# Kernel tuning notes

Measured on AMD Instinct MI355X. Metric: run time of the kernel, lower is better.

Reference implementation:

```python
import jax, jax.numpy as jnp
import numpy as np

B, S, E, H = 2, 2048, 1024, 16
D = E // H  # head_dim
SCALE = 1.0 / np.sqrt(D)


def rope_tables(seq_len, dim, dtype=jnp.float32):
    # matches RotaryEmbedding: inv_freq over even indices, emb = cat([freqs, freqs])
    inv_freq = 1.0 / (10000.0 ** (jnp.arange(0, dim, 2, dtype=dtype) / dim))
    t = jnp.arange(seq_len, dtype=dtype)
    freqs = t[:, None] * inv_freq[None, :]          # [S, D/2]
    emb = jnp.concatenate([freqs, freqs], axis=-1)  # [S, D]
    return jnp.cos(emb)[None, None], jnp.sin(emb)[None, None]  # [1,1,S,D]


def apply_rope(x, cos, sin):
    # x: [B,H,S,D]; interleaved rotate exactly as the torch code:
    # x2 = stack([-x[...,1::2], x[...,0::2]], -1).reshape_as(x)
    x2 = jnp.stack([-x[..., 1::2], x[..., 0::2]], axis=-1).reshape(x.shape)
    return x * cos + x2 * sin


def setup_inputs() -> dict:
    key = jax.random.key(0)
    ks = jax.random.split(key, 12)
    std = 1.0 / np.sqrt(E)
    inp = {
        "query": jax.random.normal(ks[0], (B, S, E), jnp.float32),
        "key": jax.random.normal(ks[1], (B, S, E), jnp.float32),
        "value": jax.random.normal(ks[2], (B, S, E), jnp.float32),
        "mask": jnp.ones((B, S), jnp.int32),
        "Wq": jax.random.normal(ks[3], (E, E), jnp.float32) * std,
        "bq": jax.random.normal(ks[4], (E,), jnp.float32) * std,
        "Wk": jax.random.normal(ks[5], (E, E), jnp.float32) * std,
        "bk": jax.random.normal(ks[6], (E,), jnp.float32) * std,
        "Wv": jax.random.normal(ks[7], (E, E), jnp.float32) * std,
        "bv": jax.random.normal(ks[8], (E,), jnp.float32) * std,
        "Wo": jax.random.normal(ks[9], (E, E), jnp.float32) * std,
        "bo": jax.random.normal(ks[10], (E,), jnp.float32) * std,
    }
    return inp


def reference(query, key, value, mask, Wq, bq, Wk, bk, Wv, bv, Wo, bo):
    b, sq, _ = query.shape
    sk = key.shape[1]
    # linear projections (torch Linear: x @ W.T + b), split into heads [B,H,S,D]
    Q = (query @ Wq.T + bq).reshape(b, sq, H, D).transpose(0, 2, 1, 3)
    K = (key @ Wk.T + bk).reshape(b, sk, H, D).transpose(0, 2, 1, 3)
    V = (value @ Wv.T + bv).reshape(b, sk, H, D).transpose(0, 2, 1, 3)
    cos_q, sin_q = rope_tables(sq, D)
    cos_k, sin_k = rope_tables(sk, D)
    Q = apply_rope(Q, cos_q, sin_q)
    K = apply_rope(K, cos_k, sin_k)
    scores = jnp.einsum("bhqd,bhkd->bhqk", Q, K) * SCALE
    neg_inf = jnp.finfo(scores.dtype).min
    scores = jnp.where(mask[:, None, None, :] == 0, neg_inf, scores)
    attn = jax.nn.softmax(scores, axis=-1)
    # dropout omitted (deterministic reference / eval mode)
    out = jnp.einsum("bhqk,bhkd->bhqd", attn, V)
    out = out.transpose(0, 2, 1, 3).reshape(b, sq, E)
    return out @ Wo.T + bo
```

## Files before the change

kernel.cpp:

```cpp
#include <hip/hip_runtime.h>
#include <stdint.h>

typedef unsigned short u16;
typedef __bf16 bf16x8 __attribute__((ext_vector_type(8)));
typedef float f32x4 __attribute__((ext_vector_type(4)));
typedef float f32x2 __attribute__((ext_vector_type(2)));
typedef u16 u16x4v __attribute__((ext_vector_type(4)));

#define DI __device__ __forceinline__

constexpr int BB = 2, SS = 2048, EE = 1024, HH = 16, DD = 64;
constexpr int MROWS = BB * SS;
constexpr int KDIM = 1024, NDIM = 1024;

constexpr float FM = 12.0f;
constexpr float MNEG = -30000.f;

DI u16 f2bf(float f) {
  uint32_t u = __float_as_uint(f);
  return (u16)((u + 0x7FFFu + ((u >> 16) & 1u)) >> 16);
}
DI float bf2f(u16 h) { return __uint_as_float(((uint32_t)h) << 16); }

DI uint32_t cvtpk_bf16(float a, float b) {
  uint32_t r;
  asm("v_cvt_pk_bf16_f32 %0, %1, %2" : "=v"(r) : "v"(a), "v"(b));
  return r;
}

DI void cp16(const void* g, void* lds) {
  __builtin_amdgcn_global_load_lds((const __attribute__((address_space(1))) void*)g,
                                   (__attribute__((address_space(3))) void*)lds, 16, 0, 0);
}

DI f32x4 mfma16(bf16x8 a, bf16x8 b, f32x4 c) {
  return __builtin_amdgcn_mfma_f32_16x16x32_bf16(a, b, c, 0, 0, 0);
}

__global__ __launch_bounds__(256) void prep_cast(
    const float* __restrict__ q, const float* __restrict__ k, const float* __restrict__ v,
    const float* __restrict__ wq, const float* __restrict__ wk, const float* __restrict__ wv,
    const float* __restrict__ wo,
    u16* __restrict__ qb, u16* __restrict__ kb, u16* __restrict__ vb,
    u16* __restrict__ wqb, u16* __restrict__ wkb, u16* __restrict__ wvb,
    u16* __restrict__ wob) {
  constexpr size_t SZI = (size_t)MROWS * EE;
  constexpr size_t SZW = (size_t)EE * EE;
  const size_t g = ((size_t)blockIdx.x * 256 + threadIdx.x) * 4;
  const float* src; u16* dst; size_t o;
  if (g < SZI)          { src = q; dst = qb; o = g; }
  else if (g < 2 * SZI) { src = k; dst = kb; o = g - SZI; }
  else if (g < 3 * SZI) { src = v; dst = vb; o = g - 2 * SZI; }
  else {
    size_t t2 = g - 3 * SZI;
    int wi = (int)(t2 / SZW);
    o = t2 - (size_t)(wi < 4 ? wi : 3) * SZW;
    src = wi == 0 ? wq : wi == 1 ? wk : wi == 2 ? wv : wo;
    dst = wi == 0 ? wqb : wi == 1 ? wkb : wi == 2 ? wvb : wob;
  }
  const float4 f = *(const float4*)(src + o);
  u16x4v hv;
  hv[0] = f2bf(f.x); hv[1] = f2bf(f.y); hv[2] = f2bf(f.z); hv[3] = f2bf(f.w);
  *(u16x4v*)(dst + o) = hv;
}

__global__ __launch_bounds__(256) void rope_tables_k(float* __restrict__ csT,
                                                     const int* __restrict__ mask,
                                                     float* __restrict__ mfl) {
  const int t = blockIdx.x * 256 + threadIdx.x;
  const int s = t >> 6, d = t & 63, j = d & 31;
  const float ang = (float)s * exp2f(-(float)j * 0.4152410118f);
  float2 cs; cs.x = cosf(ang); cs.y = sinf(ang);
  ((float2*)csT)[t] = cs;
  if (t < BB * SS) mfl[t] = mask[t] ? -FM : MNEG;
}

__global__ __launch_bounds__(256) void gemm_qkv(
    const u16* __restrict__ qb, const u16* __restrict__ kb, const u16* __restrict__ vb,
    const u16* __restrict__ wqb, const u16* __restrict__ wkb, const u16* __restrict__ wvb,
    const float* __restrict__ bq, const float* __restrict__ bk, const float* __restrict__ bv,
    u16* __restrict__ Qp, u16* __restrict__ Kp, u16* __restrict__ Vtg,
    const float* __restrict__ csT) {
  __shared__ alignas(16) u16 sA[128 * 64];
  __shared__ alignas(16) u16 sB[128 * 64];
  const int tsel = blockIdx.y >> 5;
  const bool vtr = (tsel == 2);
  const u16* A    = tsel == 0 ? wqb : tsel == 1 ? wkb : vb;
  const u16* Bm   = tsel == 0 ? qb  : tsel == 1 ? kb  : wvb;
  const float* bias = tsel == 0 ? bq : tsel == 1 ? bk : bv;

  const int fBase = blockIdx.x * 128;
  const int tBase = (blockIdx.y & 31) * 128;
  const int aBase = vtr ? tBase : fBase;
  const int bBase = vtr ? fBase : tBase;
  const int tid = threadIdx.x;
  const int lane = tid & 63, w = tid >> 6;
  const int quad = lane >> 4, l16 = lane & 15;
  const int wr = w >> 1, wc = w & 1;

  size_t aSrc[4], bSrc[4];
  u16 *aDst[4], *bDst[4];
#pragma unroll
  for (int j = 0; j < 4; ++j) {
    const int c = tid + j * 256;
    const int row = c >> 3, sl = c & 7;
    const size_t off = (size_t)row * KDIM + ((sl ^ (row & 7)) * 8);
    aSrc[j] = (size_t)aBase * KDIM + off; aDst[j] = &sA[c * 8];
    bSrc[j] = (size_t)bBase * KDIM + off; bDst[j] = &sB[c * 8];
  }

  f32x4 acc[4][4];
#pragma unroll
  for (int mi = 0; mi < 4; ++mi)
#pragma unroll
    for (int ni = 0; ni < 4; ++ni)
#pragma unroll
      for (int e = 0; e < 4; ++e) acc[mi][ni][e] = 0.f;

  const int arow = wr * 64 + l16, brow = wc * 64 + l16;

  for (int k0 = 0; k0 < KDIM; k0 += 64) {
    __syncthreads();
#pragma unroll
    for (int j = 0; j < 4; ++j) {
      cp16(A + aSrc[j] + k0, aDst[j]);
      cp16(Bm + bSrc[j] + k0, bDst[j]);
    }
    __syncthreads();
#pragma unroll
    for (int h = 0; h < 2; ++h) {
      bf16x8 af[4], bf[4];
#pragma unroll
      for (int i = 0; i < 4; ++i) {
        const int ar = arow + i * 16, br = brow + i * 16;
        af[i] = *(const bf16x8*)&sA[ar * 64 + (((h * 4 + quad) ^ (ar & 7)) << 3)];
        bf[i] = *(const bf16x8*)&sB[br * 64 + (((h * 4 + quad) ^ (br & 7)) << 3)];
      }
#pragma unroll
      for (int mi = 0; mi < 4; ++mi)
#pragma unroll
        for (int ni = 0; ni < 4; ++ni)
          acc[mi][ni] = mfma16(af[mi], bf[ni], acc[mi][ni]);
    }
  }

  if (!vtr) {
    u16* C = tsel == 0 ? Qp : Kp;
#pragma unroll
    for (int mi = 0; mi < 4; ++mi) {
      const int fm = fBase + wr * 64 + mi * 16 + quad * 4;
      const float4 b4 = *(const float4*)&bias[fm];
      const int d0 = fm & 63;
#pragma unroll
      for (int ni = 0; ni < 4; ++ni) {
        const int t = tBase + wc * 64 + ni * 16 + l16;
        const int srow = t & (SS - 1);
        const float* cs = &csT[(size_t)((srow << 6) + d0) * 2];
        const float4 cs01 = *(const float4*)cs;
        const float4 cs23 = *(const float4*)(cs + 4);
        const float v0 = acc[mi][ni][0] + b4.x;
        const float v1 = acc[mi][ni][1] + b4.y;
        const float v2 = acc[mi][ni][2] + b4.z;
        const float v3 = acc[mi][ni][3] + b4.w;
        const float o0 = v0 * cs01.x - v1 * cs01.y;
        const float o1 = v1 * cs01.z + v0 * cs01.w;
        const float o2 = v2 * cs23.x - v3 * cs23.y;
        const float o3 = v3 * cs23.z + v2 * cs23.w;
        uint2 pk;
        pk.x = cvtpk_bf16(o0, o1);
        pk.y = cvtpk_bf16(o2, o3);
        *(uint2*)&C[(size_t)t * NDIM + fm] = pk;
      }
    }
  } else {
#pragma unroll
    for (int ni = 0; ni < 4; ++ni) {
      const int f = fBase + wc * 64 + ni * 16 + l16;
      const int h = f >> 6, d = f & 63;
      const float bb = bias[f];
#pragma unroll
      for (int mi = 0; mi < 4; ++mi) {
        const int t0 = tBase + wr * 64 + mi * 16 + quad * 4;
        const int b = t0 >> 11, s0 = t0 & (SS - 1);
        const int sp0 = (s0 & ~31) | (((s0 >> 2) & 3) << 3) | (((s0 >> 4) & 1) << 2);
        uint2 pk;
        pk.x = cvtpk_bf16(acc[mi][ni][0] + bb, acc[mi][ni][1] + bb);
        pk.y = cvtpk_bf16(acc[mi][ni][2] + bb, acc[mi][ni][3] + bb);
        *(uint2*)&Vtg[((size_t)((b * 16 + h) * 64 + d)) * SS + sp0] = pk;
      }
    }
  }
}

__global__ __launch_bounds__(512, 4) void attn_kernel(
    const u16* __restrict__ Qp, const u16* __restrict__ Kp, const u16* __restrict__ Vtg,
    const float* __restrict__ mfl, u16* __restrict__ Oh) {
  __shared__ alignas(16) u16 sK[2][128 * 64];
  __shared__ alignas(16) u16 sVt[2][64 * 128];
  __shared__ alignas(16) float sMaskAll[SS];
  const int tid = threadIdx.x, lane = tid & 63, w = tid >> 6;
  const int quad = lane >> 4, l16 = lane & 15;
  const int bh = blockIdx.y, b = bh >> 4, h = bh & 15;
  const int q0 = blockIdx.x * 128 + w * 16;
  const u16* Qb = Qp + (size_t)b * SS * EE + h * DD;
  const u16* Kb = Kp + (size_t)b * SS * EE + h * DD;
  const u16* Vb = Vtg + (size_t)bh * DD * SS;
  constexpr float C1 = 0.18033688011112042f;

  bf16x8 qf[2];
#pragma unroll
  for (int ks = 0; ks < 2; ++ks)
    qf[ks] = *(const bf16x8*)(Qb + (size_t)(q0 + l16) * EE + ks * 32 + quad * 8);

  f32x4 oacc[4];
#pragma unroll
  for (int nd = 0; nd < 4; ++nd)
#pragma unroll
    for (int e = 0; e < 4; ++e) oacc[nd][e] = 0.f;
  f32x2 sum2 = {0.f, 0.f};

  auto stage = [&](int kt, int bi) {
    const int key0 = kt * 128;
#pragma unroll
    for (int i = 0; i < 2; ++i) {
      const int c = i * 512 + tid;
      const int key = c >> 3;
      const int g8 = ((c & 7) ^ (key & 7)) * 8;
      cp16(Kb + (size_t)(key0 + key) * EE + g8, &sK[bi][c * 8]);
    }
#pragma unroll
    for (int i = 0; i < 2; ++i) {
      const int L = i * 512 + tid;
      const int d = L >> 4;
      const int g8 = ((L & 15) ^ (d & 15)) * 8;
      cp16(Vb + (size_t)d * SS + key0 + g8, &sVt[bi][L * 8]);
    }
  };

  auto compute = [&](int kt, int bi) {
    const int key0 = kt * 128;
    f32x4 sacc[8];
#pragma unroll
    for (int ni = 0; ni < 8; ++ni)
#pragma unroll
      for (int e = 0; e < 4; ++e) sacc[ni][e] = 0.f;
    __builtin_amdgcn_s_setprio(1);
#pragma unroll
    for (int ks = 0; ks < 2; ++ks)
#pragma unroll
      for (int ni = 0; ni < 8; ++ni) {
        const int row = ni * 16 + l16;
        const bf16x8 kf = *(const bf16x8*)&sK[bi][row * 64 + (((ks * 4 + quad) ^ (l16 & 7)) << 3)];
        sacc[ni] = mfma16(kf, qf[ks], sacc[ni]);
      }
    __builtin_amdgcn_s_setprio(0);

    uint32_t pw32[4][4];
#pragma unroll
    for (int ni = 0; ni < 8; ++ni) {
      const int kb4 = key0 + ni * 16 + quad * 4;
      const f32x2 m01 = *(const f32x2*)&sMaskAll[kb4];
      const f32x2 m23 = *(const f32x2*)&sMaskAll[kb4 + 2];
      f32x2 t01, t23;
      t01.x = sacc[ni][0]; t01.y = sacc[ni][1];
      t23.x = sacc[ni][2]; t23.y = sacc[ni][3];
      t01 = t01 * C1 + m01;
      t23 = t23 * C1 + m23;
      f32x2 p01, p23;
      p01.x = exp2f(t01.x); p01.y = exp2f(t01.y);
      p23.x = exp2f(t23.x); p23.y = exp2f(t23.y);
      sum2 += p01;
      sum2 += p23;
      const int k2 = ni >> 1, j2 = (ni & 1) * 2;
      pw32[k2][j2]     = cvtpk_bf16(p01.x, p01.y);
      pw32[k2][j2 + 1] = cvtpk_bf16(p23.x, p23.y);
    }

    __builtin_amdgcn_s_setprio(1);
#pragma unroll
    for (int k2 = 0; k2 < 4; ++k2) {
      union { uint32_t u[4]; bf16x8 v; } pf;
#pragma unroll
      for (int j = 0; j < 4; ++j) pf.u[j] = pw32[k2][j];
#pragma unroll
      for (int nd = 0; nd < 4; ++nd) {
        const int row = nd * 16 + l16;
        const bf16x8 vf = *(const bf16x8*)&sVt[bi][row * 128 + (((k2 * 4 + quad) ^ l16) << 3)];
        oacc[nd] = mfma16(pf.v, vf, oacc[nd]);
      }
    }
    __builtin_amdgcn_s_setprio(0);
  };

  stage(0, 0);
  cp16(mfl + (size_t)b * SS + tid * 4, &sMaskAll[tid * 4]);
  __syncthreads();

  for (int kt = 0; kt < SS / 128; kt += 2) {
    if (kt + 1 < SS / 128) stage(kt + 1, 1);
    compute(kt, 0);
    __syncthreads();
    if (kt + 2 < SS / 128) stage(kt + 2, 0);
    compute(kt + 1, 1);
    __syncthreads();
  }

  float lrow = sum2.x + sum2.y;
  lrow += __shfl_xor(lrow, 16, 64);
  lrow += __shfl_xor(lrow, 32, 64);
  const float linv = lrow > 0.f ? 1.0f / lrow : 0.f;

#pragma unroll
  for (int r = 0; r < 4; ++r) {
    const float li = __shfl(linv, quad * 4 + r, 16);
    const size_t row = (size_t)(b * SS + q0 + quad * 4 + r) * EE + h * DD;
#pragma unroll
    for (int nd = 0; nd < 4; ++nd) {
      const int d = nd * 16 + l16;
      Oh[row + d] = f2bf(oacc[nd][r] * li);
    }
  }
}

__global__ __launch_bounds__(256) void gemm_out(
    const u16* __restrict__ Ab, const u16* __restrict__ Bb,
    const float* __restrict__ bias, float* __restrict__ Cout) {
  __shared__ alignas(16) u16 sA[128 * 64];
  __shared__ alignas(16) u16 sB[64 * 64];
  const int rowBase = blockIdx.y * 128;
  const int colBase = blockIdx.x * 64;
  const int tid = threadIdx.x;
  const int lane = tid & 63, w = tid >> 6;
  const int quad = lane >> 4, l16 = lane & 15;
  const int wr = w >> 1, wc = w & 1;

  size_t aSrc[4]; u16* aDst[4];
  size_t bSrc[2]; u16* bDst[2];
#pragma unroll
  for (int j = 0; j < 4; ++j) {
    const int c = tid + j * 256;
    const int row = c >> 3, sl = c & 7;
    aSrc[j] = (size_t)(rowBase + row) * KDIM + ((sl ^ (row & 7)) * 8);
    aDst[j] = &sA[c * 8];
  }
#pragma unroll
  for (int j = 0; j < 2; ++j) {
    const int c = tid + j * 256;
    const int row = c >> 3, sl = c & 7;
    bSrc[j] = (size_t)(colBase + row) * KDIM + ((sl ^ (row & 7)) * 8);
    bDst[j] = &sB[c * 8];
  }

  f32x4 acc[4][2];
#pragma unroll
  for (int mi = 0; mi < 4; ++mi)
#pragma unroll
    for (int ni = 0; ni < 2; ++ni)
#pragma unroll
      for (int e = 0; e < 4; ++e) acc[mi][ni][e] = 0.f;

  const int arow = wr * 64 + l16, brow = wc * 32 + l16;

  for (int k0 = 0; k0 < KDIM; k0 += 64) {
    __syncthreads();
#pragma unroll
    for (int j = 0; j < 4; ++j) cp16(Ab + aSrc[j] + k0, aDst[j]);
#pragma unroll
    for (int j = 0; j < 2; ++j) cp16(Bb + bSrc[j] + k0, bDst[j]);
    __syncthreads();
#pragma unroll
    for (int h = 0; h < 2; ++h) {
      bf16x8 af[4], bf[2];
#pragma unroll
      for (int i = 0; i < 4; ++i) {
        const int ar = arow + i * 16;
        af[i] = *(const bf16x8*)&sA[ar * 64 + (((h * 4 + quad) ^ (ar & 7)) << 3)];
      }
#pragma unroll
      for (int i = 0; i < 2; ++i) {
        const int br = brow + i * 16;
        bf[i] = *(const bf16x8*)&sB[br * 64 + (((h * 4 + quad) ^ (br & 7)) << 3)];
      }
#pragma unroll
      for (int mi = 0; mi < 4; ++mi)
#pragma unroll
        for (int ni = 0; ni < 2; ++ni)
          acc[mi][ni] = mfma16(af[mi], bf[ni], acc[mi][ni]);
    }
  }

#pragma unroll
  for (int mi = 0; mi < 4; ++mi) {
    const int rb = rowBase + wr * 64 + mi * 16 + quad * 4;
#pragma unroll
    for (int ni = 0; ni < 2; ++ni) {
      const int col = colBase + wc * 32 + ni * 16 + l16;
      const float bb = bias[col];
#pragma unroll
      for (int r = 0; r < 4; ++r)
        Cout[(size_t)(rb + r) * NDIM + col] = acc[mi][ni][r] + bb;
    }
  }
}

extern "C" void kernel_launch(void* const* d_in, const int* in_sizes, int n_in,
                              void* d_out, int out_size, void* d_ws, size_t ws_size,
                              hipStream_t stream) {
  const float* q    = (const float*)d_in[0];
  const float* k    = (const float*)d_in[1];
  const float* v    = (const float*)d_in[2];
  const int*   mask = (const int*)d_in[3];
  const float* Wq = (const float*)d_in[4];
  const float* bq = (const float*)d_in[5];
  const float* Wk = (const float*)d_in[6];
  const float* bk = (const float*)d_in[7];
  const float* Wv = (const float*)d_in[8];
  const float* bv = (const float*)d_in[9];
  const float* Wo = (const float*)d_in[10];
  const float* bo = (const float*)d_in[11];
  float* out = (float*)d_out;
  char* ws = (char*)d_ws;
  constexpr size_t MB = 1024 * 1024;
  u16* qb  = (u16*)(ws + 0 * MB);
  u16* kb  = (u16*)(ws + 8 * MB);
  u16* vb  = (u16*)(ws + 16 * MB);
  u16* wqb = (u16*)(ws + 24 * MB);
  u16* wkb = (u16*)(ws + 26 * MB);
  u16* wvb = (u16*)(ws + 28 * MB);
  u16* wob = (u16*)(ws + 30 * MB);
  u16* Qp  = (u16*)(ws + 32 * MB);
  u16* Kp  = (u16*)(ws + 40 * MB);
  u16* Vtg = (u16*)(ws + 48 * MB);
  u16* oh  = (u16*)(ws + 56 * MB);
  float* csT = (float*)(ws + 64 * MB);
  float* mfl = out;

  prep_cast<<<16384, 256, 0, stream>>>(q, k, v, Wq, Wk, Wv, Wo,
                                       qb, kb, vb, wqb, wkb, wvb, wob);
  rope_tables_k<<<512, 256, 0, stream>>>(csT, mask, mfl);
  gemm_qkv<<<dim3(8, 96), 256, 0, stream>>>(qb, kb, vb, wqb, wkb, wvb,
                                            bq, bk, bv, Qp, Kp, Vtg, csT);
  attn_kernel<<<dim3(16, 32), 512, 0, stream>>>(Qp, Kp, Vtg, mfl, oh);
  gemm_out<<<dim3(16, 32), 256, 0, stream>>>(oh, wob, bo, out);
}
```

Before: 250.4 us.

## Double-buffer LDS tiles in QKV and output GEMMs, use native exp2

Both projection GEMMs now use two LDS buffers, so the next K-tile is loaded while MFMAs run on the current one, and each iteration needs one barrier instead of two. The MFMA block is wrapped in setprio raises. The attention softmax also swaps exp2f for the hardware exp2 builtin, which skips the library range handling. The cost is double the LDS per block, which may lower occupancy, plus slightly different exp precision for very negative inputs.

```diff
diff --git a/kernel.cpp b/kernel.cpp
--- a/kernel.cpp
+++ b/kernel.cpp
@@ -81,8 +81,8 @@
     const float* __restrict__ bq, const float* __restrict__ bk, const float* __restrict__ bv,
     u16* __restrict__ Qp, u16* __restrict__ Kp, u16* __restrict__ Vtg,
     const float* __restrict__ csT) {
-  __shared__ alignas(16) u16 sA[128 * 64];
-  __shared__ alignas(16) u16 sB[128 * 64];
+  __shared__ alignas(16) u16 sA[2][128 * 64];
+  __shared__ alignas(16) u16 sB[2][128 * 64];
   const int tsel = blockIdx.y >> 5;
   const bool vtr = (tsel == 2);
   const u16* A    = tsel == 0 ? wqb : tsel == 1 ? wkb : vb;
@@ -99,14 +99,15 @@
   const int wr = w >> 1, wc = w & 1;
 
   size_t aSrc[4], bSrc[4];
-  u16 *aDst[4], *bDst[4];
+  int dOff[4];
 #pragma unroll
   for (int j = 0; j < 4; ++j) {
     const int c = tid + j * 256;
     const int row = c >> 3, sl = c & 7;
     const size_t off = (size_t)row * KDIM + ((sl ^ (row & 7)) * 8);
-    aSrc[j] = (size_t)aBase * KDIM + off; aDst[j] = &sA[c * 8];
-    bSrc[j] = (size_t)bBase * KDIM + off; bDst[j] = &sB[c * 8];
+    aSrc[j] = (size_t)aBase * KDIM + off;
+    bSrc[j] = (size_t)bBase * KDIM + off;
+    dOff[j] = c * 8;
   }
 
   f32x4 acc[4][4];
@@ -119,22 +120,28 @@
 
   const int arow = wr * 64 + l16, brow = wc * 64 + l16;
 
+  auto stage = [&](int k0, int bi) {
+#pragma unroll
+    for (int j = 0; j < 4; ++j) {
+      cp16(A + aSrc[j] + k0, &sA[bi][dOff[j]]);
+      cp16(Bm + bSrc[j] + k0, &sB[bi][dOff[j]]);
+    }
+  };
+
+  stage(0, 0);
+  __syncthreads();
+  int buf = 0;
   for (int k0 = 0; k0 < KDIM; k0 += 64) {
-    __syncthreads();
-#pragma unroll
-    for (int j = 0; j < 4; ++j) {
-      cp16(A + aSrc[j] + k0, aDst[j]);
-      cp16(Bm + bSrc[j] + k0, bDst[j]);
-    }
-    __syncthreads();
+    if (k0 + 64 < KDIM) stage(k0 + 64, buf ^ 1);
+    __builtin_amdgcn_s_setprio(1);
 #pragma unroll
     for (int h = 0; h < 2; ++h) {
       bf16x8 af[4], bf[4];
 #pragma unroll
       for (int i = 0; i < 4; ++i) {
         const int ar = arow + i * 16, br = brow + i * 16;
-        af[i] = *(const bf16x8*)&sA[ar * 64 + (((h * 4 + quad) ^ (ar & 7)) << 3)];
-        bf[i] = *(const bf16x8*)&sB[br * 64 + (((h * 4 + quad) ^ (br & 7)) << 3)];
+        af[i] = *(const bf16x8*)&sA[buf][ar * 64 + (((h * 4 + quad) ^ (ar & 7)) << 3)];
+        bf[i] = *(const bf16x8*)&sB[buf][br * 64 + (((h * 4 + quad) ^ (br & 7)) << 3)];
       }
 #pragma unroll
       for (int mi = 0; mi < 4; ++mi)
@@ -142,6 +149,9 @@
         for (int ni = 0; ni < 4; ++ni)
           acc[mi][ni] = mfma16(af[mi], bf[ni], acc[mi][ni]);
     }
+    __builtin_amdgcn_s_setprio(0);
+    __syncthreads();
+    buf ^= 1;
   }
 
   if (!vtr) {
@@ -267,8 +277,8 @@
       t01 = t01 * C1 + m01;
       t23 = t23 * C1 + m23;
       f32x2 p01, p23;
-      p01.x = exp2f(t01.x); p01.y = exp2f(t01.y);
-      p23.x = exp2f(t23.x); p23.y = exp2f(t23.y);
+      p01.x = __builtin_amdgcn_exp2f(t01.x); p01.y = __builtin_amdgcn_exp2f(t01.y);
+      p23.x = __builtin_amdgcn_exp2f(t23.x); p23.y = __builtin_amdgcn_exp2f(t23.y);
       sum2 += p01;
       sum2 += p23;
       const int k2 = ni >> 1, j2 = (ni & 1) * 2;
@@ -325,8 +335,8 @@
 __global__ __launch_bounds__(256) void gemm_out(
     const u16* __restrict__ Ab, const u16* __restrict__ Bb,
     const float* __restrict__ bias, float* __restrict__ Cout) {
-  __shared__ alignas(16) u16 sA[128 * 64];
-  __shared__ alignas(16) u16 sB[64 * 64];
+  __shared__ alignas(16) u16 sA[2][128 * 64];
+  __shared__ alignas(16) u16 sB[2][64 * 64];
   const int rowBase = blockIdx.y * 128;
   const int colBase = blockIdx.x * 64;
   const int tid = threadIdx.x;
@@ -334,21 +344,21 @@
   const int quad = lane >> 4, l16 = lane & 15;
   const int wr = w >> 1, wc = w & 1;
 
-  size_t aSrc[4]; u16* aDst[4];
-  size_t bSrc[2]; u16* bDst[2];
+  size_t aSrc[4]; int aOff[4];
+  size_t bSrc[2]; int bOff[2];
 #pragma unroll
   for (int j = 0; j < 4; ++j) {
     const int c = tid + j * 256;
     const int row = c >> 3, sl = c & 7;
     aSrc[j] = (size_t)(rowBase + row) * KDIM + ((sl ^ (row & 7)) * 8);
-    aDst[j] = &sA[c * 8];
+    aOff[j] = c * 8;
   }
 #pragma unroll
   for (int j = 0; j < 2; ++j) {
     const int c = tid + j * 256;
     const int row = c >> 3, sl = c & 7;
     bSrc[j] = (size_t)(colBase + row) * KDIM + ((sl ^ (row & 7)) * 8);
-    bDst[j] = &sB[c * 8];
+    bOff[j] = c * 8;
   }
 
   f32x4 acc[4][2];
@@ -361,25 +371,31 @@
 
   const int arow = wr * 64 + l16, brow = wc * 32 + l16;
 
+  auto stage = [&](int k0, int bi) {
+#pragma unroll
+    for (int j = 0; j < 4; ++j) cp16(Ab + aSrc[j] + k0, &sA[bi][aOff[j]]);
+#pragma unroll
+    for (int j = 0; j < 2; ++j) cp16(Bb + bSrc[j] + k0, &sB[bi][bOff[j]]);
+  };
+
+  stage(0, 0);
+  __syncthreads();
+  int buf = 0;
   for (int k0 = 0; k0 < KDIM; k0 += 64) {
-    __syncthreads();
-#pragma unroll
-    for (int j = 0; j < 4; ++j) cp16(Ab + aSrc[j] + k0, aDst[j]);
-#pragma unroll
-    for (int j = 0; j < 2; ++j) cp16(Bb + bSrc[j] + k0, bDst[j]);
-    __syncthreads();
+    if (k0 + 64 < KDIM) stage(k0 + 64, buf ^ 1);
+    __builtin_amdgcn_s_setprio(1);
 #pragma unroll
     for (int h = 0; h < 2; ++h) {
       bf16x8 af[4], bf[2];
 #pragma unroll
       for (int i = 0; i < 4; ++i) {
         const int ar = arow + i * 16;
-        af[i] = *(const bf16x8*)&sA[ar * 64 + (((h * 4 + quad) ^ (ar & 7)) << 3)];
+        af[i] = *(const bf16x8*)&sA[buf][ar * 64 + (((h * 4 + quad) ^ (ar & 7)) << 3)];
       }
 #pragma unroll
       for (int i = 0; i < 2; ++i) {
         const int br = brow + i * 16;
-        bf[i] = *(const bf16x8*)&sB[br * 64 + (((h * 4 + quad) ^ (br & 7)) << 3)];
+        bf[i] = *(const bf16x8*)&sB[buf][br * 64 + (((h * 4 + quad) ^ (br & 7)) << 3)];
       }
 #pragma unroll
       for (int mi = 0; mi < 4; ++mi)
@@ -387,6 +403,9 @@
         for (int ni = 0; ni < 2; ++ni)
           acc[mi][ni] = mfma16(af[mi], bf[ni], acc[mi][ni]);
     }
+    __builtin_amdgcn_s_setprio(0);
+    __syncthreads();
+    buf ^= 1;
   }
 
 #pragma unroll
```

New measurement: 229.5 us. 8.3% less time.
